# Kernel tuning notes

Hardware: AMD Instinct MI355X
Metric: run time of the kernel (lower is better)

The kernel has to match this reference:

```python
import jax, jax.numpy as jnp
import numpy as np

DIM = 256
HEADS = 8
AGENT = 16
H = W = 64
B = 8


def _trunc_normal(key, shape, std=0.02):
    return jnp.clip(std * jax.random.normal(key, shape), -2 * std, 2 * std)


def setup_inputs() -> dict:
    key = jax.random.key(0)
    ks = jax.random.split(key, 16)
    c = DIM
    return {
        "input1": jax.random.normal(ks[0], (B, c, H, W), jnp.float32),
        "input2": jax.random.normal(ks[1], (B, c, H, W), jnp.float32),
        "guidmap": jax.random.normal(ks[2], (B, 1, H, W), jnp.float32),
        "kv_w": jax.random.normal(ks[3], (c, 2 * c), jnp.float32) * (c ** -0.5),
        "kv_b": jnp.zeros((2 * c,), jnp.float32),
        "q_w": jax.random.normal(ks[4], (1, c), jnp.float32),
        "q_b": jnp.zeros((c,), jnp.float32),
        "proj_w": jax.random.normal(ks[5], (c, c), jnp.float32) * (c ** -0.5),
        "proj_b": jnp.zeros((c,), jnp.float32),
        "dwc_w": jax.random.normal(ks[6], (c, 1, 3, 3), jnp.float32) * (1.0 / 3.0),
        "dwc_b": jnp.zeros((c,), jnp.float32),
        "an_bias": _trunc_normal(ks[7], (HEADS, AGENT, 4, 4)),
        "na_bias": _trunc_normal(ks[8], (HEADS, AGENT, 4, 4)),
        "ah_bias": _trunc_normal(ks[9], (1, HEADS, AGENT, H, 1)),
        "aw_bias": _trunc_normal(ks[10], (1, HEADS, AGENT, 1, W)),
        "ha_bias": _trunc_normal(ks[11], (1, HEADS, H, 1, AGENT)),
        "wa_bias": _trunc_normal(ks[12], (1, HEADS, 1, W, AGENT)),
    }


def _dwconv(v_img, dwc_w, dwc_b):
    # depthwise 3x3, padding 1 (groups = C)
    out = jax.lax.conv_general_dilated(
        v_img, dwc_w, window_strides=(1, 1), padding=((1, 1), (1, 1)),
        feature_group_count=v_img.shape[1],
        dimension_numbers=("NCHW", "OIHW", "NCHW"))
    return out + dwc_b[None, :, None, None]


def reference(input1, input2, guidmap, kv_w, kv_b, q_w, q_b, proj_w, proj_b,
              dwc_w, dwc_b, an_bias, na_bias, ah_bias, aw_bias, ha_bias, wa_bias):
    b, c, h, w = input1.shape
    n = h * w
    nh = an_bias.shape[0]
    A = an_bias.shape[1]
    hd = c // nh
    scale = hd ** -0.5
    ps = int(A ** 0.5)  # pool size (4)

    x1 = input1.reshape(b, c, n).transpose(0, 2, 1)   # (b,n,c)
    x2 = input2.reshape(b, c, n).transpose(0, 2, 1)
    g = guidmap.reshape(b, 1, n).transpose(0, 2, 1)   # (b,n,1)

    kv1 = x1 @ kv_w + kv_b
    k1, v1 = kv1[..., :c], kv1[..., c:]
    kv2 = x2 @ kv_w + kv_b
    k2, v2 = kv2[..., :c], kv2[..., c:]
    q = g @ q_w + q_b                                  # (b,n,c)

    # adaptive avg pool of q image to (ps, ps) -> agent tokens
    q_img = q.reshape(b, h, w, c)
    agent = q_img.reshape(b, ps, h // ps, ps, w // ps, c).mean(axis=(2, 4))  # (b,ps,ps,c)
    agent = agent.reshape(b, A, nh, hd).transpose(0, 2, 1, 3)                # (b,nh,A,hd)

    def heads(t):
        return t.reshape(b, n, nh, hd).transpose(0, 2, 1, 3)  # (b,nh,n,hd)

    qh, k1h, v1h, k2h, v2h = heads(q), heads(k1), heads(v1), heads(k2), heads(v2)

    # agent -> kv position bias: bilinear upsample (align_corners=False) + axial
    pb1 = jax.image.resize(an_bias, (nh, A, h, w), method="linear").reshape(1, nh, A, n)
    pb2 = (ah_bias + aw_bias).reshape(1, nh, A, n)
    pos_bias = pb1 + pb2

    attn1 = jax.nn.softmax((agent * scale) @ jnp.swapaxes(k1h, -2, -1) + pos_bias, axis=-1)
    agent_v1 = attn1 @ v1h                                    # (b,nh,A,hd)
    attn2 = jax.nn.softmax((agent * scale) @ jnp.swapaxes(k2h, -2, -1) + pos_bias, axis=-1)
    agent_v2 = attn2 @ v2h

    # query -> agent bias
    ab1 = jax.image.resize(na_bias, (nh, A, h, w), method="linear").reshape(1, nh, A, n)
    ab1 = ab1.transpose(0, 1, 3, 2)                           # (1,nh,n,A)
    ab2 = (ha_bias + wa_bias).reshape(1, nh, n, A)
    agent_bias = ab1 + ab2

    q_attn = jax.nn.softmax((qh * scale) @ jnp.swapaxes(agent, -2, -1) + agent_bias, axis=-1)
    out1 = (q_attn @ agent_v1).transpose(0, 2, 1, 3).reshape(b, n, c)
    out2 = (q_attn @ agent_v2).transpose(0, 2, 1, 3).reshape(b, n, c)

    v1_img = v1.reshape(b, h, w, c).transpose(0, 3, 1, 2)
    v2_img = v2.reshape(b, h, w, c).transpose(0, 3, 1, 2)
    out1 = out1 + _dwconv(v1_img, dwc_w, dwc_b).reshape(b, c, n).transpose(0, 2, 1)
    out2 = out2 + _dwconv(v2_img, dwc_w, dwc_b).reshape(b, c, n).transpose(0, 2, 1)

    out1 = out1 @ proj_w + proj_b
    out2 = out2 @ proj_w + proj_b
    o1 = out1.transpose(0, 2, 1).reshape(b, c, h, w) + input1
    o2 = out2.transpose(0, 2, 1).reshape(b, c, h, w) + input2
    return (o1, o2)
```

## Files before the change

### kernel.cpp

```cpp
#include <hip/hip_runtime.h>
#include <hip/hip_bf16.h>
#include <cstddef>

#define B_   8
#define C_   256
#define HH   64
#define WW   64
#define NPOS 4096
#define NH   8
#define HD   32
#define NA   16
#define NHA  128
#define SCALE 0.17677669529663687f

typedef unsigned short u16;
typedef __attribute__((ext_vector_type(8))) short bf16x8;
typedef __attribute__((ext_vector_type(4))) float f32x4;

__device__ __forceinline__ float bfbits2f(u16 u) {
  union { unsigned int i; float f; } x; x.i = ((unsigned int)u) << 16; return x.f;
}
__device__ __forceinline__ u16 f2bfbits(float f) {
  union { float f; unsigned int i; } x; x.f = f;
  unsigned int r = x.i + 0x7fffu + ((x.i >> 16) & 1u);
  return (u16)(r >> 16);
}

__global__ __launch_bounds__(256) void k_agent(const float* __restrict__ g,
                                               const float* __restrict__ q_w,
                                               const float* __restrict__ q_b,
                                               float* __restrict__ agent_buf) {
  const int b = blockIdx.x;
  const int t = threadIdx.x;
  __shared__ float red[256];
  __shared__ float gb[16];
  const int ag = t >> 4, sub = t & 15;
  const int p1 = ag >> 2, p2 = ag & 3;
  const int y = p1 * 16 + sub, x0 = p2 * 16;
  const float* gp = g + (size_t)b * NPOS + y * WW + x0;
  float s = 0.f;
#pragma unroll
  for (int i = 0; i < 16; ++i) s += gp[i];
  red[t] = s;
  __syncthreads();
  if (sub == 0) {
    float tot = 0.f;
    for (int i = 0; i < 16; ++i) tot += red[(ag << 4) + i];
    gb[ag] = tot * (1.0f / 256.0f);
  }
  __syncthreads();
  for (int idx = t; idx < NA * C_; idx += 256) {
    const int a = idx >> 8, ci = idx & 255;
    const int h = ci >> 5, d = ci & 31;
    agent_buf[(((size_t)b * NH + h) * NA + a) * HD + d] = gb[a] * q_w[ci] + q_b[ci];
  }
}

__global__ __launch_bounds__(256) void k_wtilde(const u16* __restrict__ Wkt, const float* __restrict__ kv_b,
                                                const float* __restrict__ agent_buf,
                                                u16* __restrict__ wt, float* __restrict__ kvbD) {
  const int h = blockIdx.x, b = blockIdx.y;
  const int t = threadIdx.x;
  __shared__ u16 Wk[32 * 256];
  __shared__ float ags[16][32];
#pragma unroll
  for (int i = 0; i < 4; ++i) {
    const int idx = t + 256 * i;
    const int r = idx >> 5, sl = idx & 31;
    *(uint4*)(Wk + r * 256 + sl * 8) = *(const uint4*)(Wkt + (size_t)(h * 32 + r) * C_ + sl * 8);
  }
#pragma unroll
  for (int i = 0; i < 2; ++i) {
    const int idx = t + 256 * i;
    const int a = idx >> 5, d = idx & 31;
    ags[a][d] = agent_buf[(((size_t)b * NH + h) * NA + a) * HD + d] * SCALE;
  }
  __syncthreads();
  const int a = t >> 4, cb = (t & 15) * 16;
  float o[16];
#pragma unroll
  for (int k = 0; k < 16; ++k) o[k] = 0.f;
  for (int d = 0; d < 32; ++d) {
    const float av = ags[a][d];
#pragma unroll
    for (int k = 0; k < 16; ++k) o[k] += av * bfbits2f(Wk[d * 256 + cb + k]);
  }
  unsigned int w[8];
#pragma unroll
  for (int q = 0; q < 8; ++q)
    w[q] = (unsigned int)f2bfbits(o[2 * q]) | ((unsigned int)f2bfbits(o[2 * q + 1]) << 16);
  u16* op = wt + ((size_t)(b * NHA + h * 16 + a)) * C_ + cb;
  *(uint4*)op = make_uint4(w[0], w[1], w[2], w[3]);
  *(uint4*)(op + 8) = make_uint4(w[4], w[5], w[6], w[7]);
  if ((t & 15) == 0) {
    float s = 0.f;
#pragma unroll
    for (int d = 0; d < 32; ++d) s += ags[a][d] * kv_b[h * 32 + d];
    kvbD[b * NHA + h * 16 + a] = s;
  }
}

__global__ __launch_bounds__(256) void k_bias(const float* __restrict__ an_b, const float* __restrict__ na_b,
                                              const float* __restrict__ ah_b, const float* __restrict__ aw_b,
                                              const float* __restrict__ ha_b, const float* __restrict__ wa_b,
                                              float* __restrict__ posbT, float* __restrict__ agb) {
  const int idx = blockIdx.x * 256 + threadIdx.x;
  const int ha = idx & 127;
  const int pos = idx >> 7;
  const int h = ha >> 4, a = ha & 15;
  const int y = pos >> 6, x = pos & 63;
  const float sy = (y + 0.5f) * 0.0625f - 0.5f;
  const float sx = (x + 0.5f) * 0.0625f - 0.5f;
  const int y0 = (int)floorf(sy);
  const int x0 = (int)floorf(sx);
  const float wy = sy - (float)y0, wx = sx - (float)x0;
  const int y0c = min(max(y0, 0), 3), y1c = min(max(y0 + 1, 0), 3);
  const int x0c = min(max(x0, 0), 3), x1c = min(max(x0 + 1, 0), 3);
  const float* an4 = an_b + ((size_t)h * NA + a) * 16;
  const float* na4 = na_b + ((size_t)h * NA + a) * 16;
  const float pa_ = (1.f - wy) * ((1.f - wx) * an4[y0c * 4 + x0c] + wx * an4[y0c * 4 + x1c]) +
                    wy * ((1.f - wx) * an4[y1c * 4 + x0c] + wx * an4[y1c * 4 + x1c]);
  const float nv_ = (1.f - wy) * ((1.f - wx) * na4[y0c * 4 + x0c] + wx * na4[y0c * 4 + x1c]) +
                    wy * ((1.f - wx) * na4[y1c * 4 + x0c] + wx * na4[y1c * 4 + x1c]);
  posbT[(size_t)pos * NHA + ha] = pa_ + ah_b[((size_t)h * NA + a) * HH + y] + aw_b[((size_t)h * NA + a) * WW + x];
  agb[((size_t)h * NPOS + pos) * NA + a] =
      nv_ + ha_b[((size_t)h * HH + y) * NA + a] + wa_b[((size_t)h * WW + x) * NA + a];
}

__global__ __launch_bounds__(256) void k_prep_in(const float* __restrict__ in1, const float* __restrict__ in2,
                                                 u16* __restrict__ At1, u16* __restrict__ At2) {
  const int z = blockIdx.z;
  const int src = z >> 3, b = z & 7;
  const float* in = src ? in2 : in1;
  u16* At = src ? At2 : At1;
  const int pos0 = blockIdx.x * 64;
  const int ci0 = blockIdx.y * 64;
  __shared__ float tile[64][68];
  const int t = threadIdx.x;
  const int rpos = (t & 15) << 2, rci = t >> 4;
#pragma unroll
  for (int i = 0; i < 4; ++i) {
    const int ci_l = rci + 16 * i;
    const float4 v = *(const float4*)(in + ((size_t)b * C_ + ci0 + ci_l) * NPOS + pos0 + rpos);
    tile[ci_l][rpos + 0] = v.x; tile[ci_l][rpos + 1] = v.y;
    tile[ci_l][rpos + 2] = v.z; tile[ci_l][rpos + 3] = v.w;
  }
  __syncthreads();
#pragma unroll
  for (int i = 0; i < 2; ++i) {
    const int u = t + 256 * i;
    const int p = u >> 3, s = u & 7;
    unsigned int w[4];
#pragma unroll
    for (int q = 0; q < 4; ++q) {
      const u16 lo = f2bfbits(tile[s * 8 + 2 * q][p]);
      const u16 hi = f2bfbits(tile[s * 8 + 2 * q + 1][p]);
      w[q] = (unsigned int)lo | ((unsigned int)hi << 16);
    }
    *(uint4*)(At + ((size_t)(pos0 + p)) * C_ + (size_t)b * NPOS * C_ + ci0 + s * 8) =
        make_uint4(w[0], w[1], w[2], w[3]);
  }
}

__global__ __launch_bounds__(256) void k_prep_w(const float* __restrict__ kv_w, const float* __restrict__ proj_w,
                                                u16* __restrict__ Wkt, u16* __restrict__ Pwt) {
  const int x = blockIdx.x;
  const float* W; u16* T; int j0, ci0, ncols;
  if (x < 32) { W = kv_w;  T = Wkt; j0 = (x & 7) * 64; ci0 = (x >> 3) * 64; ncols = 512; }
  else        { W = proj_w; T = Pwt; j0 = ((x - 32) & 3) * 64; ci0 = ((x - 32) >> 2) * 64; ncols = 256; }
  __shared__ float tile[64][68];
  const int t = threadIdx.x;
  const int rj = (t & 15) << 2, rci = t >> 4;
#pragma unroll
  for (int i = 0; i < 4; ++i) {
    const int ci_l = rci + 16 * i;
    const float4 v = *(const float4*)(W + (size_t)(ci0 + ci_l) * ncols + j0 + rj);
    tile[ci_l][rj + 0] = v.x; tile[ci_l][rj + 1] = v.y;
    tile[ci_l][rj + 2] = v.z; tile[ci_l][rj + 3] = v.w;
  }
  __syncthreads();
#pragma unroll
  for (int i = 0; i < 2; ++i) {
    const int u = t + 256 * i;
    const int p = u >> 3, s = u & 7;
    unsigned int w[4];
#pragma unroll
    for (int q = 0; q < 4; ++q) {
      const u16 lo = f2bfbits(tile[s * 8 + 2 * q][p]);
      const u16 hi = f2bfbits(tile[s * 8 + 2 * q + 1][p]);
      w[q] = (unsigned int)lo | ((unsigned int)hi << 16);
    }
    *(uint4*)(T + (size_t)(j0 + p) * C_ + ci0 + s * 8) = make_uint4(w[0], w[1], w[2], w[3]);
  }
}

__global__ __launch_bounds__(256) void k_v_mfma(const u16* __restrict__ At1, const u16* __restrict__ At2,
                                                const u16* __restrict__ Wkt, const float* __restrict__ kv_b,
                                                u16* __restrict__ v1, u16* __restrict__ v2) {
  const int z = blockIdx.z;
  const int src = z >> 3, b = z & 7;
  const u16* At = src ? At2 : At1;
  u16* vout = src ? v2 : v1;
  const int pos0 = blockIdx.x * 128;
  const int j0 = blockIdx.y * 128;

  __shared__ __align__(16) u16 SM[16384];
  u16* Ab = SM;
  u16* Bb = SM + 8192;

  const int t = threadIdx.x;
  const int wave = t >> 6, lane = t & 63;
  const int wm = wave >> 1, wn = wave & 1;
  const int g = lane >> 4;

  const u16* Ag = Wkt + (size_t)(256 + j0) * C_;
  const u16* Bg = At + ((size_t)b * NPOS + pos0) * C_;

  f32x4 acc[4][4];
#pragma unroll
  for (int m = 0; m < 4; ++m)
#pragma unroll
    for (int n = 0; n < 4; ++n) { acc[m][n][0]=0.f; acc[m][n][1]=0.f; acc[m][n][2]=0.f; acc[m][n][3]=0.f; }

  uint4 ra[4], rb[4];
#define V_LOAD(KT)                                                         \
  _Pragma("unroll") for (int i = 0; i < 4; ++i) {                          \
    const int u = t + 256 * i, rr = u >> 3, ss = u & 7;                    \
    ra[i] = *(const uint4*)(Ag + (size_t)rr * C_ + (KT) * 64 + ss * 8);    \
    rb[i] = *(const uint4*)(Bg + (size_t)rr * C_ + (KT) * 64 + ss * 8);    \
  }
#define V_WRITE()                                                          \
  _Pragma("unroll") for (int i = 0; i < 4; ++i) {                          \
    const int u = t + 256 * i, rr = u >> 3, ss = u & 7;                    \
    const int sw = ((ss ^ (rr & 7)) << 3);                                 \
    *(uint4*)(Ab + rr * 64 + sw) = ra[i];                                  \
    *(uint4*)(Bb + rr * 64 + sw) = rb[i];                                  \
  }

  V_LOAD(0);
  V_WRITE();
  V_LOAD(1);
  __syncthreads();

  for (int kt = 0; kt < 4; ++kt) {
#pragma unroll
    for (int kk = 0; kk < 2; ++kk) {
      bf16x8 af[4], bfr[4];
#pragma unroll
      for (int m = 0; m < 4; ++m) {
        const int r = wm * 64 + m * 16 + (lane & 15);
        af[m] = *(const bf16x8*)(Ab + r * 64 + (((kk * 4 + g) ^ (r & 7)) << 3));
      }
#pragma unroll
      for (int n = 0; n < 4; ++n) {
        const int c = wn * 64 + n * 16 + (lane & 15);
        bfr[n] = *(const bf16x8*)(Bb + c * 64 + (((kk * 4 + g) ^ (c & 7)) << 3));
      }
#pragma unroll
      for (int m = 0; m < 4; ++m)
#pragma unroll
        for (int n = 0; n < 4; ++n)
          acc[m][n] = __builtin_amdgcn_mfma_f32_16x16x32_bf16(af[m], bfr[n], acc[m][n], 0, 0, 0);
    }
    if (kt < 3) {
      __syncthreads();
      V_WRITE();
      if (kt < 2) V_LOAD(kt + 2);
      __syncthreads();
    }
  }
#undef V_LOAD
#undef V_WRITE

  __syncthreads();
#pragma unroll
  for (int m = 0; m < 4; ++m) {
    const int jl = wm * 64 + m * 16 + (lane >> 4) * 4;
    const float4 bv = *(const float4*)(kv_b + 256 + j0 + jl);
#pragma unroll
    for (int n = 0; n < 4; ++n) {
      const int pos_l = wn * 64 + n * 16 + (lane & 15);
      const f32x4 a = acc[m][n];
      ushort4 st;
      st.x = f2bfbits(a[0] + bv.x); st.y = f2bfbits(a[1] + bv.y);
      st.z = f2bfbits(a[2] + bv.z); st.w = f2bfbits(a[3] + bv.w);
      const int slot = (jl >> 3) ^ (pos_l & 7);
      *(ushort4*)(SM + pos_l * 128 + slot * 8 + (jl & 7)) = st;
    }
  }
  __syncthreads();
#pragma unroll
  for (int i = 0; i < 8; ++i) {
    const int idx = t + 256 * i;
    const int row = idx >> 4, sl = idx & 15;
    const uint4 v = *(const uint4*)(SM + row * 128 + ((sl ^ (row & 7)) << 3));
    *(uint4*)(vout + ((size_t)b * NPOS + pos0 + row) * C_ + j0 + sl * 8) = v;
  }
}

__global__ __launch_bounds__(256) void k_score(const u16* __restrict__ At1, const u16* __restrict__ At2,
                                               const u16* __restrict__ wt, const float* __restrict__ posbT,
                                               const float* __restrict__ kvbD,
                                               u16* __restrict__ E, float* __restrict__ lsumP) {
  const int z = blockIdx.z;
  const int src = z >> 3, b = z & 7;
  const int sb = src * 8 + b;
  const u16* At = src ? At2 : At1;
  const int pos0 = blockIdx.x * 128;

  __shared__ __align__(16) u16 SM[16384];
  __shared__ float lsum_sm[2][128];
  u16* Ab = SM;
  u16* Bb = SM + 8192;

  const int t = threadIdx.x;
  const int wave = t >> 6, lane = t & 63;
  const int wm = wave >> 1, wn = wave & 1;
  const int g = lane >> 4;

  const u16* Ag = At + ((size_t)b * NPOS + pos0) * C_;
  const u16* Bg = wt + (size_t)b * NHA * C_;

  f32x4 acc[4][4];
#pragma unroll
  for (int m = 0; m < 4; ++m)
#pragma unroll
    for (int n = 0; n < 4; ++n) { acc[m][n][0]=0.f; acc[m][n][1]=0.f; acc[m][n][2]=0.f; acc[m][n][3]=0.f; }

  uint4 ra[4], rb[4];
#define S_LOAD(KT)                                                         \
  _Pragma("unroll") for (int i = 0; i < 4; ++i) {                          \
    const int u = t + 256 * i, rr = u >> 3, ss = u & 7;                    \
    ra[i] = *(const uint4*)(Ag + (size_t)rr * C_ + (KT) * 64 + ss * 8);    \
    rb[i] = *(const uint4*)(Bg + (size_t)rr * C_ + (KT) * 64 + ss * 8);    \
  }
#define S_WRITE()                                                          \
  _Pragma("unroll") for (int i = 0; i < 4; ++i) {                          \
    const int u = t + 256 * i, rr = u >> 3, ss = u & 7;                    \
    const int sw = ((ss ^ (rr & 7)) << 3);                                 \
    *(uint4*)(Ab + rr * 64 + sw) = ra[i];                                  \
    *(uint4*)(Bb + rr * 64 + sw) = rb[i];                                  \
  }

  S_LOAD(0);
  S_WRITE();
  S_LOAD(1);
  __syncthreads();

  for (int kt = 0; kt < 4; ++kt) {
#pragma unroll
    for (int kk = 0; kk < 2; ++kk) {
      bf16x8 af[4], bfr[4];
#pragma unroll
      for (int m = 0; m < 4; ++m) {
        const int r = wm * 64 + m * 16 + (lane & 15);
        af[m] = *(const bf16x8*)(Ab + r * 64 + (((kk * 4 + g) ^ (r & 7)) << 3));
      }
#pragma unroll
      for (int n = 0; n < 4; ++n) {
        const int c = wn * 64 + n * 16 + (lane & 15);
        bfr[n] = *(const bf16x8*)(Bb + c * 64 + (((kk * 4 + g) ^ (c & 7)) << 3));
      }
#pragma unroll
      for (int m = 0; m < 4; ++m)
#pragma unroll
        for (int n = 0; n < 4; ++n)
          acc[m][n] = __builtin_amdgcn_mfma_f32_16x16x32_bf16(af[m], bfr[n], acc[m][n], 0, 0, 0);
    }
    if (kt < 3) {
      __syncthreads();
      S_WRITE();
      if (kt < 2) S_LOAD(kt + 2);
      __syncthreads();
    }
  }
#undef S_LOAD
#undef S_WRITE

  __syncthreads();
  float ls[4] = {0.f, 0.f, 0.f, 0.f};
#pragma unroll
  for (int n = 0; n < 4; ++n) {
    const int ha_l = wn * 64 + n * 16 + (lane & 15);
    const float kb = kvbD[b * NHA + ha_l];
#pragma unroll
    for (int m = 0; m < 4; ++m) {
      const int pos_l = wm * 64 + m * 16 + (lane >> 4) * 4;
      float e[4];
#pragma unroll
      for (int j = 0; j < 4; ++j) {
        const float s = acc[m][n][j] + posbT[(size_t)(pos0 + pos_l + j) * NHA + ha_l] + kb;
        e[j] = __expf(s);
        ls[n] += e[j];
      }
      ushort4 st;
      st.x = f2bfbits(e[0]); st.y = f2bfbits(e[1]); st.z = f2bfbits(e[2]); st.w = f2bfbits(e[3]);
      const int sw = (pos_l >> 3) ^ (ha_l & 15);
      *(ushort4*)(SM + ha_l * 128 + sw * 8 + (pos_l & 7)) = st;
    }
  }
#pragma unroll
  for (int n = 0; n < 4; ++n) {
    float v = ls[n];
    v += __shfl_xor(v, 16);
    v += __shfl_xor(v, 32);
    ls[n] = v;
  }
  if (lane < 16) {
#pragma unroll
    for (int n = 0; n < 4; ++n) lsum_sm[wm][wn * 64 + n * 16 + lane] = ls[n];
  }
  __syncthreads();
  if (t < 128)
    lsumP[((size_t)sb * 32 + blockIdx.x) * NHA + t] = lsum_sm[0][t] + lsum_sm[1][t];
#pragma unroll
  for (int i = 0; i < 8; ++i) {
    const int idx = t + 256 * i;
    const int row = idx >> 4, sl = idx & 15;
    const uint4 v = *(const uint4*)(SM + row * 128 + ((sl ^ (row & 15)) << 3));
    *(uint4*)(E + ((size_t)sb * NHA + row) * NPOS + pos0 + sl * 8) = v;
  }
}

__global__ __launch_bounds__(256) void k_pv(const float* __restrict__ in1, const float* __restrict__ in2,
                                            const u16* __restrict__ E, float* __restrict__ T_p) {
  const int kc = blockIdx.x;
  const int ci0 = blockIdx.y * 128;
  const int sb = blockIdx.z;
  const int src = sb >> 3, b = sb & 7;
  const float* in = src ? in2 : in1;
  const int kpos0 = kc * 512;

  __shared__ __align__(16) u16 As[8192];
  __shared__ __align__(16) u16 Bs[8192];

  const int t = threadIdx.x;
  const int wave = t >> 6, lane = t & 63;
  const int wm = wave >> 1, wn = wave & 1;
  const int g = lane >> 4;

  const float* Ain = in + (size_t)b * C_ * NPOS;
  const u16* Eg = E + (size_t)sb * NHA * NPOS;

  f32x4 acc[4][4];
#pragma unroll
  for (int m = 0; m < 4; ++m)
#pragma unroll
    for (int n = 0; n < 4; ++n) { acc[m][n][0]=0.f; acc[m][n][1]=0.f; acc[m][n][2]=0.f; acc[m][n][3]=0.f; }

  float4 pa[8];
  uint4 pb[4];
#define PV_LOAD(KT)                                                            \
  _Pragma("unroll") for (int i = 0; i < 8; ++i) {                              \
    const int idx = t + 256 * i, rr = idx >> 4, fq = idx & 15;                 \
    pa[i] = *(const float4*)(Ain + (size_t)(ci0 + rr) * NPOS + kpos0 + (KT) * 64 + fq * 4); \
  }                                                                            \
  _Pragma("unroll") for (int i = 0; i < 4; ++i) {                              \
    const int idx = t + 256 * i, rr = idx >> 3, ss = idx & 7;                  \
    pb[i] = *(const uint4*)(Eg + (size_t)rr * NPOS + kpos0 + (KT) * 64 + ss * 8); \
  }
#define PV_WRITE()                                                             \
  _Pragma("unroll") for (int i = 0; i < 8; ++i) {                              \
    const int idx = t + 256 * i, rr = idx >> 4, fq = idx & 15;                 \
    ushort4 st;                                                                \
    st.x = f2bfbits(pa[i].x); st.y = f2bfbits(pa[i].y);                        \
    st.z = f2bfbits(pa[i].z); st.w = f2bfbits(pa[i].w);                        \
    const int sw = ((fq >> 1) ^ (rr & 7));                                     \
    *(ushort4*)(As + rr * 64 + sw * 8 + (fq & 1) * 4) = st;                    \
  }                                                                            \
  _Pragma("unroll") for (int i = 0; i < 4; ++i) {                              \
    const int idx = t + 256 * i, rr = idx >> 3, ss = idx & 7;                  \
    *(uint4*)(Bs + rr * 64 + ((ss ^ (rr & 7)) << 3)) = pb[i];                  \
  }

  PV_LOAD(0);
  PV_WRITE();
  PV_LOAD(1);
  __syncthreads();

  for (int kt = 0; kt < 8; ++kt) {
#pragma unroll
    for (int kk = 0; kk < 2; ++kk) {
      bf16x8 af[4], bfr[4];
#pragma unroll
      for (int m = 0; m < 4; ++m) {
        const int r = wm * 64 + m * 16 + (lane & 15);
        af[m] = *(const bf16x8*)(As + r * 64 + (((kk * 4 + g) ^ (r & 7)) << 3));
      }
#pragma unroll
      for (int n = 0; n < 4; ++n) {
        const int c = wn * 64 + n * 16 + (lane & 15);
        bfr[n] = *(const bf16x8*)(Bs + c * 64 + (((kk * 4 + g) ^ (c & 7)) << 3));
      }
#pragma unroll
      for (int m = 0; m < 4; ++m)
#pragma unroll
        for (int n = 0; n < 4; ++n)
          acc[m][n] = __builtin_amdgcn_mfma_f32_16x16x32_bf16(af[m], bfr[n], acc[m][n], 0, 0, 0);
    }
    if (kt < 7) {
      __syncthreads();
      PV_WRITE();
      if (kt < 6) PV_LOAD(kt + 2);
      __syncthreads();
    }
  }
#undef PV_LOAD
#undef PV_WRITE

#pragma unroll
  for (int m = 0; m < 4; ++m) {
    const int ci_l = wm * 64 + m * 16 + (lane >> 4) * 4;
#pragma unroll
    for (int n = 0; n < 4; ++n) {
      const int ha_l = wn * 64 + n * 16 + (lane & 15);
      const f32x4 a = acc[m][n];
      *(float4*)(T_p + (((size_t)sb * 8 + kc) * NHA + ha_l) * C_ + ci0 + ci_l) =
          make_float4(a[0], a[1], a[2], a[3]);
    }
  }
}

__global__ __launch_bounds__(256) void k_agentv(const float* __restrict__ T_p, const float* __restrict__ lsumP,
                                                const u16* __restrict__ Wkt, const float* __restrict__ kv_b,
                                                float* __restrict__ agent_v) {
  const int h = blockIdx.x, sb = blockIdx.y;
  const int t = threadIdx.x;
  __shared__ float Tred[16 * 256];
  __shared__ u16 Wv[32 * 256];
  __shared__ float lsum_s[16];
#pragma unroll
  for (int i = 0; i < 4; ++i) {
    const int idx = t + 256 * i;
    const int r = idx >> 5, sl = idx & 31;
    *(uint4*)(Wv + r * 256 + sl * 8) = *(const uint4*)(Wkt + (size_t)(256 + h * 32 + r) * C_ + sl * 8);
  }
#pragma unroll
  for (int i = 0; i < 16; ++i) {
    const int idx = t + 256 * i;
    const int a = idx >> 8, ci = idx & 255;
    float s = 0.f;
#pragma unroll
    for (int kc = 0; kc < 8; ++kc)
      s += T_p[(((size_t)sb * 8 + kc) * NHA + h * 16 + a) * C_ + ci];
    Tred[a * 256 + ci] = s;
  }
  if (t < 16) {
    float s = 0.f;
#pragma unroll
    for (int pt = 0; pt < 32; ++pt) s += lsumP[((size_t)sb * 32 + pt) * NHA + h * 16 + t];
    lsum_s[t] = s;
  }
  __syncthreads();
  const int a = t >> 4, dp = (t & 15) * 2;
  float o0 = 0.f, o1 = 0.f;
  const float* Tr = Tred + a * 256;
  for (int ci = 0; ci < 256; ++ci) {
    const float tv = Tr[ci];
    o0 += tv * bfbits2f(Wv[dp * 256 + ci]);
    o1 += tv * bfbits2f(Wv[(dp + 1) * 256 + ci]);
  }
  const float inv = 1.0f / lsum_s[a];
  float* op = agent_v + (size_t)sb * NHA * HD + (h * 16 + a) * HD + dp;
  op[0] = o0 * inv + kv_b[256 + h * 32 + dp];
  op[1] = o1 * inv + kv_b[256 + h * 32 + dp + 1];
}

__global__ __launch_bounds__(256) void k_qattn(const float* __restrict__ g,
                                               const float* __restrict__ q_w, const float* __restrict__ q_b,
                                               const float* __restrict__ agent_buf,
                                               const float* __restrict__ agent_v,
                                               const float* __restrict__ agb,
                                               u16* __restrict__ o1s, u16* __restrict__ o2s) {
  const int h = blockIdx.y, b = blockIdx.z;
  const int t = threadIdx.x;
  const int pos = blockIdx.x * 256 + t;
  __shared__ float dotW[16], dotB[16];
  __shared__ float av1[16][32], av2[16][32];
  for (int idx = t; idx < 512; idx += 256) {
    const int a = idx >> 5, d = idx & 31;
    av1[a][d] = agent_v[(size_t)b * NHA * HD + (h * 16 + a) * HD + d];
    av2[a][d] = agent_v[(size_t)(8 + b) * NHA * HD + (h * 16 + a) * HD + d];
  }
  if (t < 16) {
    float dw = 0.f, db = 0.f;
    const float* agp = agent_buf + (((size_t)b * NH + h) * NA + t) * HD;
#pragma unroll
    for (int d = 0; d < HD; ++d) {
      const float ad = agp[d];
      dw += ad * q_w[h * HD + d];
      db += ad * q_b[h * HD + d];
    }
    dotW[t] = dw * SCALE;
    dotB[t] = db * SCALE;
  }
  __syncthreads();
  const float gv = g[(size_t)b * NPOS + pos];
  const float* abp = agb + ((size_t)h * NPOS + pos) * NA;
  float s[16];
  float m = -1e30f;
#pragma unroll
  for (int a = 0; a < 16; ++a) {
    s[a] = gv * dotW[a] + dotB[a] + abp[a];
    m = fmaxf(m, s[a]);
  }
  float l = 0.f;
#pragma unroll
  for (int a = 0; a < 16; ++a) {
    s[a] = __expf(s[a] - m);
    l += s[a];
  }
  const float inv = 1.0f / l;
  float o1[32] = {}, o2[32] = {};
#pragma unroll
  for (int a = 0; a < 16; ++a) {
    const float pa = s[a] * inv;
#pragma unroll
    for (int d = 0; d < 32; ++d) {
      o1[d] += pa * av1[a][d];
      o2[d] += pa * av2[a][d];
    }
  }
  u16* o1p = o1s + ((size_t)b * NPOS + pos) * C_ + h * HD;
  u16* o2p = o2s + ((size_t)b * NPOS + pos) * C_ + h * HD;
#pragma unroll
  for (int blk = 0; blk < 4; ++blk) {
    unsigned int w1[4], w2[4];
#pragma unroll
    for (int q = 0; q < 4; ++q) {
      w1[q] = (unsigned int)f2bfbits(o1[blk * 8 + 2 * q]) | ((unsigned int)f2bfbits(o1[blk * 8 + 2 * q + 1]) << 16);
      w2[q] = (unsigned int)f2bfbits(o2[blk * 8 + 2 * q]) | ((unsigned int)f2bfbits(o2[blk * 8 + 2 * q + 1]) << 16);
    }
    *(uint4*)(o1p + blk * 8) = make_uint4(w1[0], w1[1], w1[2], w1[3]);
    *(uint4*)(o2p + blk * 8) = make_uint4(w2[0], w2[1], w2[2], w2[3]);
  }
}

__global__ __launch_bounds__(256) void k_dwconv(const u16* __restrict__ v1, const u16* __restrict__ v2,
                                                const float* __restrict__ dwc_w, const float* __restrict__ dwc_b,
                                                u16* __restrict__ o1s, u16* __restrict__ o2s) {
  const u16* V = blockIdx.z ? v2 : v1;
  u16* out = blockIdx.z ? o2s : o1s;
  const int b = blockIdx.y;
  const int ci = threadIdx.x;
  const int pos0 = blockIdx.x << 3;
  float w[9];
#pragma unroll
  for (int q = 0; q < 9; ++q) w[q] = dwc_w[ci * 9 + q];
  const float bias = dwc_b[ci];
  const u16* vb = V + (size_t)b * NPOS * C_ + ci;
  for (int pp = 0; pp < 8; ++pp) {
    const int pos = pos0 + pp;
    const int y = pos >> 6, x = pos & 63;
    float acc = bias;
#pragma unroll
    for (int dy = -1; dy <= 1; ++dy) {
      const int yy = y + dy;
      if (yy < 0 || yy > 63) continue;
#pragma unroll
      for (int dx = -1; dx <= 1; ++dx) {
        const int xx = x + dx;
        if (xx < 0 || xx > 63) continue;
        acc += w[(dy + 1) * 3 + (dx + 1)] * bfbits2f(vb[(size_t)(yy * 64 + xx) * C_]);
      }
    }
    const size_t oidx = ((size_t)b * NPOS + pos) * C_ + ci;
    out[oidx] = f2bfbits(bfbits2f(out[oidx]) + acc);
  }
}

__global__ __launch_bounds__(256) void k_proj_mfma(const u16* __restrict__ o1s, const u16* __restrict__ o2s,
                                                   const u16* __restrict__ Pwt, const float* __restrict__ proj_b,
                                                   const float* __restrict__ in1, const float* __restrict__ in2,
                                                   float* __restrict__ out1, float* __restrict__ out2) {
  const int z = blockIdx.z;
  const int src = z >> 3, b = z & 7;
  const u16* S = src ? o2s : o1s;
  const float* inp = src ? in2 : in1;
  float* outp = src ? out2 : out1;
  const int pos0 = blockIdx.x * 128;
  const int co0 = blockIdx.y * 128;

  __shared__ __align__(16) u16 SM[16384];
  u16* Ab = SM;
  u16* Bb = SM + 8192;
  float* SMF = (float*)SM;

  const int t = threadIdx.x;
  const int wave = t >> 6, lane = t & 63;
  const int wm = wave >> 1, wn = wave & 1;
  const int g = lane >> 4;

  const u16* Ag = S + ((size_t)b * NPOS + pos0) * C_;
  const u16* Bg = Pwt + (size_t)co0 * C_;

  f32x4 acc[4][4];
#pragma unroll
  for (int m = 0; m < 4; ++m)
#pragma unroll
    for (int n = 0; n < 4; ++n) { acc[m][n][0]=0.f; acc[m][n][1]=0.f; acc[m][n][2]=0.f; acc[m][n][3]=0.f; }

  uint4 ra[4], rb[4];
#define PJ_LOAD(KT)                                                        \
  _Pragma("unroll") for (int i = 0; i < 4; ++i) {                          \
    const int u = t + 256 * i, rr = u >> 3, ss = u & 7;                    \
    ra[i] = *(const uint4*)(Ag + (size_t)rr * C_ + (KT) * 64 + ss * 8);    \
    rb[i] = *(const uint4*)(Bg + (size_t)rr * C_ + (KT) * 64 + ss * 8);    \
  }
#define PJ_WRITE()                                                         \
  _Pragma("unroll") for (int i = 0; i < 4; ++i) {                          \
    const int u = t + 256 * i, rr = u >> 3, ss = u & 7;                    \
    const int sw = ((ss ^ (rr & 7)) << 3);                                 \
    *(uint4*)(Ab + rr * 64 + sw) = ra[i];                                  \
    *(uint4*)(Bb + rr * 64 + sw) = rb[i];                                  \
  }

  PJ_LOAD(0);
  PJ_WRITE();
  PJ_LOAD(1);
  __syncthreads();

  for (int kt = 0; kt < 4; ++kt) {
#pragma unroll
    for (int kk = 0; kk < 2; ++kk) {
      bf16x8 af[4], bfr[4];
#pragma unroll
      for (int m = 0; m < 4; ++m) {
        const int r = wm * 64 + m * 16 + (lane & 15);
        af[m] = *(const bf16x8*)(Ab + r * 64 + (((kk * 4 + g) ^ (r & 7)) << 3));
      }
#pragma unroll
      for (int n = 0; n < 4; ++n) {
        const int c = wn * 64 + n * 16 + (lane & 15);
        bfr[n] = *(const bf16x8*)(Bb + c * 64 + (((kk * 4 + g) ^ (c & 7)) << 3));
      }
#pragma unroll
      for (int m = 0; m < 4; ++m)
#pragma unroll
        for (int n = 0; n < 4; ++n)
          acc[m][n] = __builtin_amdgcn_mfma_f32_16x16x32_bf16(af[m], bfr[n], acc[m][n], 0, 0, 0);
    }
    if (kt < 3) {
      __syncthreads();
      PJ_WRITE();
      if (kt < 2) PJ_LOAD(kt + 2);
      __syncthreads();
    }
  }
#undef PJ_LOAD
#undef PJ_WRITE

#pragma unroll
  for (int hf = 0; hf < 2; ++hf) {
    __syncthreads();
    if (wn == hf) {
#pragma unroll
      for (int n = 0; n < 4; ++n) {
        const int co_l = n * 16 + (lane & 15);
#pragma unroll
        for (int m = 0; m < 4; ++m) {
          const int pos_l = wm * 64 + m * 16 + (lane >> 4) * 4;
          const int slot = (pos_l >> 2) ^ (co_l & 7);
          const f32x4 a = acc[m][n];
          *(float4*)(SMF + co_l * 128 + slot * 4) = make_float4(a[0], a[1], a[2], a[3]);
        }
      }
    }
    __syncthreads();
#pragma unroll
    for (int i = 0; i < 8; ++i) {
      const int idx = t + 256 * i;
      const int row = idx >> 5, sl = idx & 31;
      const float4 v = *(const float4*)(SMF + row * 128 + ((sl ^ (row & 7)) << 2));
      const int co = co0 + hf * 64 + row;
      const float pb = proj_b[co];
      const size_t base = ((size_t)b * C_ + co) * NPOS + pos0 + sl * 4;
      const float4 res = *(const float4*)(inp + base);
      *(float4*)(outp + base) = make_float4(v.x + pb + res.x, v.y + pb + res.y,
                                            v.z + pb + res.z, v.w + pb + res.w);
    }
  }
}

extern "C" void kernel_launch(void* const* d_in, const int* in_sizes, int n_in,
                              void* d_out, int out_size, void* d_ws, size_t ws_size,
                              hipStream_t stream) {
  const float* input1 = (const float*)d_in[0];
  const float* input2 = (const float*)d_in[1];
  const float* guid   = (const float*)d_in[2];
  const float* kv_w   = (const float*)d_in[3];
  const float* kv_b   = (const float*)d_in[4];
  const float* q_w    = (const float*)d_in[5];
  const float* q_b    = (const float*)d_in[6];
  const float* proj_w = (const float*)d_in[7];
  const float* proj_b = (const float*)d_in[8];
  const float* dwc_w  = (const float*)d_in[9];
  const float* dwc_b  = (const float*)d_in[10];
  const float* an_b   = (const float*)d_in[11];
  const float* na_b   = (const float*)d_in[12];
  const float* ah_b   = (const float*)d_in[13];
  const float* aw_b   = (const float*)d_in[14];
  const float* ha_b   = (const float*)d_in[15];
  const float* wa_b   = (const float*)d_in[16];

  char* W = (char*)d_ws;
  u16* At1 = (u16*)W;        W += (size_t)B_ * NPOS * C_ * 2;
  u16* At2 = (u16*)W;        W += (size_t)B_ * NPOS * C_ * 2;
  u16* v1  = (u16*)W;        W += (size_t)B_ * NPOS * C_ * 2;
  u16* v2  = (u16*)W;        W += (size_t)B_ * NPOS * C_ * 2;
  u16* o1s = (u16*)W;        W += (size_t)B_ * NPOS * C_ * 2;
  u16* o2s = (u16*)W;        W += (size_t)B_ * NPOS * C_ * 2;
  u16* E   = (u16*)W;        W += (size_t)16 * NHA * NPOS * 2;
  float* T_p = (float*)W;    W += (size_t)16 * 8 * NHA * C_ * 4;
  u16* Wkt = (u16*)W;        W += (size_t)512 * C_ * 2;
  u16* Pwt = (u16*)W;        W += (size_t)C_ * C_ * 2;
  u16* wt  = (u16*)W;        W += (size_t)B_ * NHA * C_ * 2;
  float* posbT = (float*)W;  W += (size_t)NPOS * NHA * 4;
  float* agb   = (float*)W;  W += (size_t)NH * NPOS * NA * 4;
  float* agentb = (float*)W; W += (size_t)B_ * NH * NA * HD * 4;
  float* kvbD   = (float*)W; W += (size_t)B_ * NHA * 4;
  float* lsumP  = (float*)W; W += (size_t)16 * 32 * NHA * 4;
  float* agent_v = (float*)W; W += (size_t)16 * NHA * HD * 4;

  float* out1 = (float*)d_out;
  float* out2 = out1 + (size_t)B_ * C_ * NPOS;

  hipLaunchKernelGGL(k_agent, dim3(B_), dim3(256), 0, stream, guid, q_w, q_b, agentb);
  hipLaunchKernelGGL(k_bias, dim3((NHA * NPOS) / 256), dim3(256), 0, stream,
                     an_b, na_b, ah_b, aw_b, ha_b, wa_b, posbT, agb);
  hipLaunchKernelGGL(k_prep_w, dim3(48), dim3(256), 0, stream, kv_w, proj_w, Wkt, Pwt);
  hipLaunchKernelGGL(k_wtilde, dim3(NH, B_), dim3(256), 0, stream, Wkt, kv_b, agentb, wt, kvbD);
  hipLaunchKernelGGL(k_prep_in, dim3(64, 4, 16), dim3(256), 0, stream, input1, input2, At1, At2);
  hipLaunchKernelGGL(k_v_mfma, dim3(32, 2, 16), dim3(256), 0, stream,
                     At1, At2, Wkt, kv_b, v1, v2);
  hipLaunchKernelGGL(k_score, dim3(32, 1, 16), dim3(256), 0, stream,
                     At1, At2, wt, posbT, kvbD, E, lsumP);
  hipLaunchKernelGGL(k_pv, dim3(8, 2, 16), dim3(256), 0, stream, input1, input2, E, T_p);
  hipLaunchKernelGGL(k_agentv, dim3(NH, 16), dim3(256), 0, stream, T_p, lsumP, Wkt, kv_b, agent_v);
  hipLaunchKernelGGL(k_qattn, dim3(NPOS / 256, NH, B_), dim3(256), 0, stream,
                     guid, q_w, q_b, agentb, agent_v, agb, o1s, o2s);
  hipLaunchKernelGGL(k_dwconv, dim3(NPOS / 8, B_, 2), dim3(256), 0, stream,
                     v1, v2, dwc_w, dwc_b, o1s, o2s);
  hipLaunchKernelGGL(k_proj_mfma, dim3(32, 2, 16), dim3(256), 0, stream,
                     o1s, o2s, Pwt, proj_b, input1, input2, out1, out2);
}
```

Before: 293.5 us.

## Vectorize depthwise conv over 8 channels and compute agent bias inline

The depthwise conv kernel now has each thread handle 8 contiguous channels of one pixel, using 16-byte loads of bf16 values and a transposed weight table prepared by a new tiny kernel. Before, each thread handled one channel with scalar 2-byte loads. Separately, the query-to-agent bias is no longer materialized as an 8x4096x16 buffer by k_bias. It is recomputed in k_qattn from the small na/ha/wa bias tensors, which removes a global write and read in exchange for extra arithmetic and small gathers per thread. One extra kernel launch is added.

```diff
diff --git a/kernel.cpp b/kernel.cpp
--- a/kernel.cpp
+++ b/kernel.cpp
@@ -25,6 +25,12 @@
   unsigned int r = x.i + 0x7fffu + ((x.i >> 16) & 1u);
   return (u16)(r >> 16);
 }
+__device__ __forceinline__ void unpack8(const uint4 v, float* f) {
+  f[0] = bfbits2f((u16)(v.x & 0xffff)); f[1] = bfbits2f((u16)(v.x >> 16));
+  f[2] = bfbits2f((u16)(v.y & 0xffff)); f[3] = bfbits2f((u16)(v.y >> 16));
+  f[4] = bfbits2f((u16)(v.z & 0xffff)); f[5] = bfbits2f((u16)(v.z >> 16));
+  f[6] = bfbits2f((u16)(v.w & 0xffff)); f[7] = bfbits2f((u16)(v.w >> 16));
+}
 
 __global__ __launch_bounds__(256) void k_agent(const float* __restrict__ g,
                                                const float* __restrict__ q_w,
@@ -100,10 +106,9 @@
   }
 }
 
-__global__ __launch_bounds__(256) void k_bias(const float* __restrict__ an_b, const float* __restrict__ na_b,
+__global__ __launch_bounds__(256) void k_bias(const float* __restrict__ an_b,
                                               const float* __restrict__ ah_b, const float* __restrict__ aw_b,
-                                              const float* __restrict__ ha_b, const float* __restrict__ wa_b,
-                                              float* __restrict__ posbT, float* __restrict__ agb) {
+                                              float* __restrict__ posbT) {
   const int idx = blockIdx.x * 256 + threadIdx.x;
   const int ha = idx & 127;
   const int pos = idx >> 7;
@@ -117,14 +122,9 @@
   const int y0c = min(max(y0, 0), 3), y1c = min(max(y0 + 1, 0), 3);
   const int x0c = min(max(x0, 0), 3), x1c = min(max(x0 + 1, 0), 3);
   const float* an4 = an_b + ((size_t)h * NA + a) * 16;
-  const float* na4 = na_b + ((size_t)h * NA + a) * 16;
   const float pa_ = (1.f - wy) * ((1.f - wx) * an4[y0c * 4 + x0c] + wx * an4[y0c * 4 + x1c]) +
                     wy * ((1.f - wx) * an4[y1c * 4 + x0c] + wx * an4[y1c * 4 + x1c]);
-  const float nv_ = (1.f - wy) * ((1.f - wx) * na4[y0c * 4 + x0c] + wx * na4[y0c * 4 + x1c]) +
-                    wy * ((1.f - wx) * na4[y1c * 4 + x0c] + wx * na4[y1c * 4 + x1c]);
   posbT[(size_t)pos * NHA + ha] = pa_ + ah_b[((size_t)h * NA + a) * HH + y] + aw_b[((size_t)h * NA + a) * WW + x];
-  agb[((size_t)h * NPOS + pos) * NA + a] =
-      nv_ + ha_b[((size_t)h * HH + y) * NA + a] + wa_b[((size_t)h * WW + x) * NA + a];
 }
 
 __global__ __launch_bounds__(256) void k_prep_in(const float* __restrict__ in1, const float* __restrict__ in2,
@@ -192,6 +192,14 @@
     }
     *(uint4*)(T + (size_t)(j0 + p) * C_ + ci0 + s * 8) = make_uint4(w[0], w[1], w[2], w[3]);
   }
+}
+
+__global__ __launch_bounds__(256) void k_prep_dwc(const float* __restrict__ dwc_w, const float* __restrict__ dwc_b,
+                                                  float* __restrict__ dwcT) {
+  const int ci = threadIdx.x;
+#pragma unroll
+  for (int q = 0; q < 9; ++q) dwcT[q * 256 + ci] = dwc_w[ci * 9 + q];
+  dwcT[9 * 256 + ci] = dwc_b[ci];
 }
 
 __global__ __launch_bounds__(256) void k_v_mfma(const u16* __restrict__ At1, const u16* __restrict__ At2,
@@ -570,7 +578,9 @@
                                                const float* __restrict__ q_w, const float* __restrict__ q_b,
                                                const float* __restrict__ agent_buf,
                                                const float* __restrict__ agent_v,
-                                               const float* __restrict__ agb,
+                                               const float* __restrict__ na_b,
+                                               const float* __restrict__ ha_b,
+                                               const float* __restrict__ wa_b,
                                                u16* __restrict__ o1s, u16* __restrict__ o2s) {
   const int h = blockIdx.y, b = blockIdx.z;
   const int t = threadIdx.x;
@@ -595,13 +605,36 @@
     dotB[t] = db * SCALE;
   }
   __syncthreads();
+  const int y = pos >> 6, x = pos & 63;
+  const float sy = (y + 0.5f) * 0.0625f - 0.5f;
+  const float sx = (x + 0.5f) * 0.0625f - 0.5f;
+  const int y0 = (int)floorf(sy);
+  const int x0 = (int)floorf(sx);
+  const float wy = sy - (float)y0, wx = sx - (float)x0;
+  const int y0c = min(max(y0, 0), 3), y1c = min(max(y0 + 1, 0), 3);
+  const int x0c = min(max(x0, 0), 3), x1c = min(max(x0 + 1, 0), 3);
+  const float c00 = (1.f - wy) * (1.f - wx), c01 = (1.f - wy) * wx;
+  const float c10 = wy * (1.f - wx), c11 = wy * wx;
+  const int i00 = y0c * 4 + x0c, i01 = y0c * 4 + x1c;
+  const int i10 = y1c * 4 + x0c, i11 = y1c * 4 + x1c;
+  float hav[16], wav[16];
+  {
+    const float* hp = ha_b + ((size_t)h * HH + y) * NA;
+    const float* wp = wa_b + ((size_t)h * WW + x) * NA;
+#pragma unroll
+    for (int q = 0; q < 4; ++q) {
+      *(float4*)(hav + 4 * q) = *(const float4*)(hp + 4 * q);
+      *(float4*)(wav + 4 * q) = *(const float4*)(wp + 4 * q);
+    }
+  }
   const float gv = g[(size_t)b * NPOS + pos];
-  const float* abp = agb + ((size_t)h * NPOS + pos) * NA;
   float s[16];
   float m = -1e30f;
 #pragma unroll
   for (int a = 0; a < 16; ++a) {
-    s[a] = gv * dotW[a] + dotB[a] + abp[a];
+    const float* na4 = na_b + ((size_t)h * NA + a) * 16;
+    const float nv = c00 * na4[i00] + c01 * na4[i01] + c10 * na4[i10] + c11 * na4[i11];
+    s[a] = gv * dotW[a] + dotB[a] + nv + hav[a] + wav[a];
     m = fmaxf(m, s[a]);
   }
   float l = 0.f;
@@ -637,36 +670,56 @@
 }
 
 __global__ __launch_bounds__(256) void k_dwconv(const u16* __restrict__ v1, const u16* __restrict__ v2,
-                                                const float* __restrict__ dwc_w, const float* __restrict__ dwc_b,
+                                                const float* __restrict__ dwcT,
                                                 u16* __restrict__ o1s, u16* __restrict__ o2s) {
   const u16* V = blockIdx.z ? v2 : v1;
   u16* out = blockIdx.z ? o2s : o1s;
   const int b = blockIdx.y;
-  const int ci = threadIdx.x;
-  const int pos0 = blockIdx.x << 3;
-  float w[9];
-#pragma unroll
-  for (int q = 0; q < 9; ++q) w[q] = dwc_w[ci * 9 + q];
-  const float bias = dwc_b[ci];
-  const u16* vb = V + (size_t)b * NPOS * C_ + ci;
-  for (int pp = 0; pp < 8; ++pp) {
-    const int pos = pos0 + pp;
-    const int y = pos >> 6, x = pos & 63;
-    float acc = bias;
-#pragma unroll
-    for (int dy = -1; dy <= 1; ++dy) {
-      const int yy = y + dy;
-      if (yy < 0 || yy > 63) continue;
-#pragma unroll
-      for (int dx = -1; dx <= 1; ++dx) {
-        const int xx = x + dx;
-        if (xx < 0 || xx > 63) continue;
-        acc += w[(dy + 1) * 3 + (dx + 1)] * bfbits2f(vb[(size_t)(yy * 64 + xx) * C_]);
-      }
-    }
-    const size_t oidx = ((size_t)b * NPOS + pos) * C_ + ci;
-    out[oidx] = f2bfbits(bfbits2f(out[oidx]) + acc);
-  }
+  const int t = threadIdx.x;
+  const int cg = t & 31;
+  const int ch = cg * 8;
+  const int px = t >> 5;
+  const int pos = (blockIdx.x << 3) + px;
+  const int y = pos >> 6, x = pos & 63;
+
+  float acc[8];
+  {
+    const float4 b0 = *(const float4*)(dwcT + 9 * 256 + ch);
+    const float4 b1 = *(const float4*)(dwcT + 9 * 256 + ch + 4);
+    acc[0] = b0.x; acc[1] = b0.y; acc[2] = b0.z; acc[3] = b0.w;
+    acc[4] = b1.x; acc[5] = b1.y; acc[6] = b1.z; acc[7] = b1.w;
+  }
+  const u16* vb = V + (size_t)b * NPOS * C_ + ch;
+#pragma unroll
+  for (int dy = -1; dy <= 1; ++dy) {
+    const int yy = y + dy;
+    if (yy < 0 || yy > 63) continue;
+#pragma unroll
+    for (int dx = -1; dx <= 1; ++dx) {
+      const int xx = x + dx;
+      if (xx < 0 || xx > 63) continue;
+      const int q = (dy + 1) * 3 + (dx + 1);
+      const float4 w0 = *(const float4*)(dwcT + q * 256 + ch);
+      const float4 w1 = *(const float4*)(dwcT + q * 256 + ch + 4);
+      const uint4 vv = *(const uint4*)(vb + (size_t)(yy * 64 + xx) * C_);
+      float f8[8];
+      unpack8(vv, f8);
+      acc[0] += w0.x * f8[0]; acc[1] += w0.y * f8[1];
+      acc[2] += w0.z * f8[2]; acc[3] += w0.w * f8[3];
+      acc[4] += w1.x * f8[4]; acc[5] += w1.y * f8[5];
+      acc[6] += w1.z * f8[6]; acc[7] += w1.w * f8[7];
+    }
+  }
+  u16* op = out + ((size_t)b * NPOS + pos) * C_ + ch;
+  const uint4 ov = *(const uint4*)op;
+  float f8[8];
+  unpack8(ov, f8);
+  unsigned int wo[4];
+#pragma unroll
+  for (int q2 = 0; q2 < 4; ++q2)
+    wo[q2] = (unsigned int)f2bfbits(f8[2 * q2] + acc[2 * q2]) |
+             ((unsigned int)f2bfbits(f8[2 * q2 + 1] + acc[2 * q2 + 1]) << 16);
+  *(uint4*)op = make_uint4(wo[0], wo[1], wo[2], wo[3]);
 }
 
 __global__ __launch_bounds__(256) void k_proj_mfma(const u16* __restrict__ o1s, const u16* __restrict__ o2s,
@@ -816,19 +869,20 @@
   u16* Pwt = (u16*)W;        W += (size_t)C_ * C_ * 2;
   u16* wt  = (u16*)W;        W += (size_t)B_ * NHA * C_ * 2;
   float* posbT = (float*)W;  W += (size_t)NPOS * NHA * 4;
-  float* agb   = (float*)W;  W += (size_t)NH * NPOS * NA * 4;
   float* agentb = (float*)W; W += (size_t)B_ * NH * NA * HD * 4;
   float* kvbD   = (float*)W; W += (size_t)B_ * NHA * 4;
   float* lsumP  = (float*)W; W += (size_t)16 * 32 * NHA * 4;
   float* agent_v = (float*)W; W += (size_t)16 * NHA * HD * 4;
+  float* dwcT    = (float*)W; W += (size_t)10 * 256 * 4;
 
   float* out1 = (float*)d_out;
   float* out2 = out1 + (size_t)B_ * C_ * NPOS;
 
   hipLaunchKernelGGL(k_agent, dim3(B_), dim3(256), 0, stream, guid, q_w, q_b, agentb);
   hipLaunchKernelGGL(k_bias, dim3((NHA * NPOS) / 256), dim3(256), 0, stream,
-                     an_b, na_b, ah_b, aw_b, ha_b, wa_b, posbT, agb);
+                     an_b, ah_b, aw_b, posbT);
   hipLaunchKernelGGL(k_prep_w, dim3(48), dim3(256), 0, stream, kv_w, proj_w, Wkt, Pwt);
+  hipLaunchKernelGGL(k_prep_dwc, dim3(1), dim3(256), 0, stream, dwc_w, dwc_b, dwcT);
   hipLaunchKernelGGL(k_wtilde, dim3(NH, B_), dim3(256), 0, stream, Wkt, kv_b, agentb, wt, kvbD);
   hipLaunchKernelGGL(k_prep_in, dim3(64, 4, 16), dim3(256), 0, stream, input1, input2, At1, At2);
   hipLaunchKernelGGL(k_v_mfma, dim3(32, 2, 16), dim3(256), 0, stream,
@@ -838,9 +892,9 @@
   hipLaunchKernelGGL(k_pv, dim3(8, 2, 16), dim3(256), 0, stream, input1, input2, E, T_p);
   hipLaunchKernelGGL(k_agentv, dim3(NH, 16), dim3(256), 0, stream, T_p, lsumP, Wkt, kv_b, agent_v);
   hipLaunchKernelGGL(k_qattn, dim3(NPOS / 256, NH, B_), dim3(256), 0, stream,
-                     guid, q_w, q_b, agentb, agent_v, agb, o1s, o2s);
+                     guid, q_w, q_b, agentb, agent_v, na_b, ha_b, wa_b, o1s, o2s);
   hipLaunchKernelGGL(k_dwconv, dim3(NPOS / 8, B_, 2), dim3(256), 0, stream,
-                     v1, v2, dwc_w, dwc_b, o1s, o2s);
+                     v1, v2, dwcT, o1s, o2s);
   hipLaunchKernelGGL(k_proj_mfma, dim3(32, 2, 16), dim3(256), 0, stream,
                      o1s, o2s, Pwt, proj_b, input1, input2, out1, out2);
 }
```

New measurement: 271.6 us. -7.5%, faster.
